# Optimization experiments

Measured on AMD Instinct MI355X. Metric: run time of the kernel, lower is better.

Reference implementation:

```python
import jax, jax.numpy as jnp
import numpy as np

B, N, D = 2, 2048, 256
H, HID, EN = 8, 64, 2
ALPHA = 0.2
NEG = -9e15


def setup_inputs() -> dict:
    key = jax.random.key(0)
    k1, k2, k3, k4, k5, k6 = jax.random.split(key, 6)
    fea_mats = jax.random.normal(k1, (B, N, D), dtype=jnp.float32)
    adj_mats = jax.random.randint(k2, (B, N, N), 0, 2).astype(jnp.float32)
    # xavier-uniform-like init (gain 1.414)
    def xav(k, shape):
        fan_in, fan_out = shape[-2], shape[-1]
        bound = 1.414 * np.sqrt(6.0 / (fan_in + fan_out))
        return jax.random.uniform(k, shape, jnp.float32, -bound, bound)
    W_att = xav(k3, (H, D, HID))          # per-head projection
    a_att = xav(k4, (H, 2 * HID, 1))      # per-head attention vector
    W_last = xav(k5, (H * HID, EN))       # last-layer projection
    a_last = xav(k6, (2 * EN, 1))         # last-layer attention vector
    return {"fea_mats": fea_mats, "adj_mats": adj_mats,
            "W_att": W_att, "a_att": a_att,
            "W_last": W_last, "a_last": a_last}


def _leaky(x):
    return jnp.where(x >= 0, x, ALPHA * x)


def _masked_attn(e, adj):
    # torch: where(adj!=0, e, 0) * adj; masked_fill(==0, -9e15); softmax(dim=1 over columns)
    att = jnp.where(adj != 0, e, jnp.zeros_like(e)) * adj
    att = jnp.where(att == 0, jnp.full_like(att, NEG), att)
    return jax.nn.softmax(att, axis=-1)


def reference(fea_mats, adj_mats, W_att, a_att, W_last, a_last):
    # ---- multi-head GAT layers (concat=True), eval mode -> dropout = identity ----
    wh = jnp.einsum('bnd,hdo->bhno', fea_mats, W_att)        # [B,H,N,HID]
    a1 = a_att[:, :HID, 0]                                   # [H,HID]
    a2 = a_att[:, HID:, 0]                                   # [H,HID]
    e1 = jnp.einsum('bhno,ho->bhn', wh, a1)                  # regulon part
    e2 = jnp.einsum('bhno,ho->bhn', wh, a2)                  # gene part
    e = _leaky(e1[:, :, :, None] + e2[:, :, None, :])        # [B,H,N,N]
    att = _masked_attn(e, adj_mats[:, None])                 # [B,H,N,N]
    x = jax.nn.elu(jnp.einsum('bhnm,bhmo->bhno', att, wh))   # [B,H,N,HID]
    x = jnp.transpose(x, (0, 2, 1, 3)).reshape(B, N, H * HID)
    # ---- last layer (concat=False), adj narrowed to square (already square) ----
    wh2 = jnp.einsum('bnd,de->bne', x, W_last)               # [B,N,EN]
    b1 = a_last[:EN, 0]
    b2 = a_last[EN:, 0]
    e = _leaky(jnp.einsum('bne,e->bn', wh2, b1)[:, :, None]
               + jnp.einsum('bne,e->bn', wh2, b2)[:, None, :])  # [B,N,N]
    att = _masked_attn(e, adj_mats)
    out = jax.nn.elu(jnp.einsum('bnm,bme->bne', att, wh2))   # [B,N,EN]
    return out
```

## Files before the change

### kernel.cpp

```cpp
#include <hip/hip_runtime.h>
#include <hip/hip_bf16.h>
#include <cstdint>
#include <cstddef>

#define B_ 2
#define N_ 2048
#define D_ 256
#define H_ 8
#define HID_ 64
#define EN_ 2
#define ALPHA 0.2f
#define NEGBIG (-3.0e38f)
#define LOG2E 1.4426950408889634f

typedef __bf16 bf16x8 __attribute__((ext_vector_type(8)));
typedef float f32x4 __attribute__((ext_vector_type(4)));
typedef unsigned short ushort8 __attribute__((ext_vector_type(8)));
typedef float float4v __attribute__((ext_vector_type(4)));
typedef float float2v __attribute__((ext_vector_type(2)));

__device__ __forceinline__ unsigned short f2bf(float f) {
    unsigned int u = __builtin_bit_cast(unsigned int, f);
    unsigned int r = u + 0x7FFFu + ((u >> 16) & 1u);
    return (unsigned short)(r >> 16);
}
__device__ __forceinline__ float bf2f(unsigned short u) {
    unsigned int x = ((unsigned int)u) << 16;
    return __builtin_bit_cast(float, x);
}
__device__ __forceinline__ float leakyf(float x) { return fmaxf(x, ALPHA * x); }

__device__ __forceinline__ ushort8 cvt8(const float* __restrict__ p) {
    float4v x0 = *(const float4v*)p;
    float4v x1 = *(const float4v*)(p + 4);
    ushort8 r;
    #pragma unroll
    for (int e = 0; e < 4; ++e) { r[e] = f2bf(x0[e]); r[e + 4] = f2bf(x1[e]); }
    return r;
}

__global__ void k_transpose_w(const float* __restrict__ W,
                              unsigned short* __restrict__ WT) {
    int h = blockIdx.x;
    const float* Wh = W + (size_t)h * D_ * HID_;
    unsigned short* WTh = WT + (size_t)h * HID_ * D_;
    for (int idx = threadIdx.x; idx < D_ * HID_; idx += blockDim.x) {
        int d = idx / HID_, o = idx % HID_;
        WTh[o * D_ + d] = f2bf(Wh[idx]);
    }
}

__global__ __launch_bounds__(256) void k_wh(
    const float* __restrict__ fea,
    const unsigned short* __restrict__ WT,
    const float* __restrict__ a_att,
    unsigned short* __restrict__ whT,
    float* __restrict__ e1, float* __restrict__ e2)
{
    int bid = blockIdx.x;
    int i0 = (bid & 31) << 6;
    int h  = (bid >> 5) & 7;
    int b  = bid >> 8;

    __shared__ __align__(16) union SmemA {
        struct { unsigned short fa[64 * 72]; unsigned short wt[64 * 72]; } s;
        float tr[64 * 65];
    } u;

    int t = threadIdx.x;
    int lane = t & 63;
    int wv = t >> 6;
    int r = lane & 15, q = lane >> 4;
    int ra = t >> 2;
    int cc = (t & 3) * 16;

    f32x4 acc[4] = {};

    const float* fearow = fea + ((size_t)(b * N_ + i0 + ra)) * D_;
    const unsigned short* wtrow = WT + ((size_t)(h * 64 + ra)) * D_;

    for (int d0 = 0; d0 < D_; d0 += 64) {
        *(ushort8*)&u.s.fa[ra * 72 + cc]     = cvt8(fearow + d0 + cc);
        *(ushort8*)&u.s.fa[ra * 72 + cc + 8] = cvt8(fearow + d0 + cc + 8);
        *(ushort8*)&u.s.wt[ra * 72 + cc]     = *(const ushort8*)(wtrow + d0 + cc);
        *(ushort8*)&u.s.wt[ra * 72 + cc + 8] = *(const ushort8*)(wtrow + d0 + cc + 8);
        __syncthreads();
        #pragma unroll
        for (int k0 = 0; k0 < 64; k0 += 32) {
            bf16x8 a = *(const bf16x8*)&u.s.fa[(16 * wv + r) * 72 + k0 + q * 8];
            #pragma unroll
            for (int f = 0; f < 4; ++f) {
                bf16x8 bb = *(const bf16x8*)&u.s.wt[(16 * f + r) * 72 + k0 + q * 8];
                acc[f] = __builtin_amdgcn_mfma_f32_16x16x32_bf16(a, bb, acc[f], 0, 0, 0);
            }
        }
        __syncthreads();
    }

    float a1v[4], a2v[4];
    #pragma unroll
    for (int f = 0; f < 4; ++f) {
        a1v[f] = a_att[h * 128 + 16 * f + r];
        a2v[f] = a_att[h * 128 + 64 + 16 * f + r];
    }
    #pragma unroll
    for (int rr = 0; rr < 4; ++rr) {
        float s1 = 0.f, s2 = 0.f;
        #pragma unroll
        for (int f = 0; f < 4; ++f) { s1 += acc[f][rr] * a1v[f]; s2 += acc[f][rr] * a2v[f]; }
        #pragma unroll
        for (int m = 1; m < 16; m <<= 1) {
            s1 += __shfl_xor(s1, m, 64);
            s2 += __shfl_xor(s2, m, 64);
        }
        if (r == 0) {
            int i = i0 + 16 * wv + 4 * q + rr;
            size_t idx = ((size_t)(b * H_ + h)) * N_ + i;
            e1[idx] = s1 * LOG2E; e2[idx] = s2 * LOG2E;
        }
    }

    #pragma unroll
    for (int f = 0; f < 4; ++f)
        #pragma unroll
        for (int rr = 0; rr < 4; ++rr)
            u.tr[(16 * f + r) * 65 + 16 * wv + 4 * q + rr] = acc[f][rr];
    __syncthreads();
    {
        int o = t >> 2;
        int ch = (t & 3) * 16;
        unsigned short tmp[16];
        #pragma unroll
        for (int e = 0; e < 16; ++e) tmp[e] = f2bf(u.tr[o * 65 + ch + e]);
        ushort8* dst = (ushort8*)(whT + (((size_t)(b * H_ + h) * 64 + o)) * N_ + i0 + ch);
        dst[0] = *(ushort8*)&tmp[0];
        dst[1] = *(ushort8*)&tmp[8];
    }
}

__global__ __launch_bounds__(256) void k_maxe2(const float* __restrict__ e2,
                                               float* __restrict__ mx) {
    int bh = blockIdx.x;
    int t = threadIdx.x;
    const float* row = e2 + (size_t)bh * N_;
    float M = NEGBIG;
    #pragma unroll
    for (int it = 0; it < N_ / 256; ++it) M = fmaxf(M, row[it * 256 + t]);
    #pragma unroll
    for (int s = 1; s < 64; s <<= 1) M = fmaxf(M, __shfl_xor(M, s, 64));
    __shared__ float red[4];
    if ((t & 63) == 0) red[t >> 6] = M;
    __syncthreads();
    if (t == 0) mx[bh] = fmaxf(fmaxf(red[0], red[1]), fmaxf(red[2], red[3]));
}

template<int JPER>
__global__ __launch_bounds__(256, 2) void k_pv1(
    const float* __restrict__ adj,
    const unsigned short* __restrict__ whT,
    const float* __restrict__ e1g, const float* __restrict__ e2g,
    const float* __restrict__ maxE2,
    unsigned short* __restrict__ x_part,
    float* __restrict__ zPart)
{
    constexpr int NT = JPER / 64;
    int s  = blockIdx.x;
    int i0 = blockIdx.y << 7;
    int bh = blockIdx.z;
    int h = bh & 7, b = bh >> 3;
    int jBeg = s * JPER;

    __shared__ __align__(16) unsigned short wt_lds[2][64 * 64];
    __shared__ float tE[JPER];
    __shared__ float vE[JPER];

    int t = threadIdx.x;
    int lane = t & 63;
    int wv = t >> 6;
    int r = lane & 15, q = lane >> 4;

    int ir0 = i0 + wv * 32 + r;
    int ir1 = ir0 + 16;
    float mx = maxE2[bh];
    float e1_0 = e1g[(size_t)bh * N_ + ir0];
    float e1_1 = e1g[(size_t)bh * N_ + ir1];
    float m0 = leakyf(e1_0 + mx), m1 = leakyf(e1_1 + mx);
    float sI0 = __builtin_amdgcn_exp2f(e1_0 - m0);
    float uI0 = __builtin_amdgcn_exp2f(ALPHA * e1_0 - m0);
    float sI1 = __builtin_amdgcn_exp2f(e1_1 - m1);
    float uI1 = __builtin_amdgcn_exp2f(ALPHA * e1_1 - m1);

    const float* e2p = e2g + (size_t)bh * N_ + jBeg;
    const float* ap0 = adj + ((size_t)(b * N_ + ir0)) * N_ + jBeg + q * 8;
    const float* ap1 = ap0 + (size_t)16 * N_;

    int c0 = t, c1 = t + 256;
    const unsigned short* wsrc0 =
        whT + ((size_t)bh * 64 + (c0 >> 3)) * N_ + jBeg + (c0 & 7) * 8;
    const unsigned short* wsrc1 =
        whT + ((size_t)bh * 64 + (c1 >> 3)) * N_ + jBeg + (c1 & 7) * 8;
    int woff0 = (c0 * 8) ^ (((c0 >> 3) & 7) << 3);
    int woff1 = (c1 * 8) ^ (((c1 >> 3) & 7) << 3);

    int swz = (r & 7) << 3;
    int koff0 = (8 * q) ^ swz;
    int koff1 = (32 + 8 * q) ^ swz;

    bf16x8 ones;
    #pragma unroll
    for (int e = 0; e < 8; ++e) ones[e] = (__bf16)1.0f;

    f32x4 acc[2][4] = {};
    f32x4 accz[2] = {};

    float4v aA[8], aB[8];
    ushort8 wN0, wN1;

#define LOADADJ(A, tile) do {                                                   \
        const float* p0 = ap0 + (tile) * 64;                                    \
        const float* p1 = ap1 + (tile) * 64;                                    \
        A[0] = *(const float4v*)(p0);      A[1] = *(const float4v*)(p0 + 4);    \
        A[2] = *(const float4v*)(p0 + 32); A[3] = *(const float4v*)(p0 + 36);   \
        A[4] = *(const float4v*)(p1);      A[5] = *(const float4v*)(p1 + 4);    \
        A[6] = *(const float4v*)(p1 + 32); A[7] = *(const float4v*)(p1 + 36);   \
    } while (0)
#define LOADW(tile) do {                                                        \
        wN0 = *(const ushort8*)(wsrc0 + (tile) * 64);                           \
        wN1 = *(const ushort8*)(wsrc1 + (tile) * 64);                           \
    } while (0)

    for (int jj = t; jj < JPER; jj += 256) {
        float ev = e2p[jj];
        tE[jj] = __builtin_amdgcn_exp2f(ev);
        vE[jj] = __builtin_amdgcn_exp2f(ALPHA * ev);
    }
    LOADW(0);
    *(ushort8*)&wt_lds[0][woff0] = wN0;
    *(ushort8*)&wt_lds[0][woff1] = wN1;
    if (NT > 1) LOADW(1);
    LOADADJ(aA, 0);
    if (NT > 1) LOADADJ(aB, 1);
    asm volatile("s_waitcnt lgkmcnt(0)" ::: "memory");
    __builtin_amdgcn_s_barrier();

    auto pgen = [&](const float4v* av, float sI, float uI,
                    const float4v& t0, const float4v& t1,
                    const float4v& t2, const float4v& t3,
                    const float4v& v0, const float4v& v1,
                    const float4v& v2, const float4v& v3,
                    bf16x8& pa0, bf16x8& pa1) {
        #pragma unroll
        for (int e = 0; e < 4; ++e) {
            pa0[e]     = (__bf16)(fmaxf(sI * t0[e], uI * v0[e]) * av[0][e]);
            pa0[e + 4] = (__bf16)(fmaxf(sI * t1[e], uI * v1[e]) * av[1][e]);
            pa1[e]     = (__bf16)(fmaxf(sI * t2[e], uI * v2[e]) * av[2][e]);
            pa1[e + 4] = (__bf16)(fmaxf(sI * t3[e], uI * v3[e]) * av[3][e]);
        }
    };

    #pragma unroll 2
    for (int t8 = 0; t8 < NT; ++t8) {
        const int cur = t8 & 1;
        if (t8 + 1 < NT) {
            *(ushort8*)&wt_lds[cur ^ 1][woff0] = wN0;
            *(ushort8*)&wt_lds[cur ^ 1][woff1] = wN1;
        }
        if (t8 + 2 < NT) LOADW(t8 + 2);

        const float* tb = &tE[t8 * 64 + q * 8];
        const float* vb = &vE[t8 * 64 + q * 8];
        float4v t0 = *(const float4v*)(tb),      t1 = *(const float4v*)(tb + 4);
        float4v t2 = *(const float4v*)(tb + 32), t3 = *(const float4v*)(tb + 36);
        float4v v0 = *(const float4v*)(vb),      v1 = *(const float4v*)(vb + 4);
        float4v v2 = *(const float4v*)(vb + 32), v3 = *(const float4v*)(vb + 36);

        bf16x8 pa00, pa01, pa10, pa11;
        if (cur == 0) {
            pgen(aA,     sI0, uI0, t0, t1, t2, t3, v0, v1, v2, v3, pa00, pa01);
            pgen(aA + 4, sI1, uI1, t0, t1, t2, t3, v0, v1, v2, v3, pa10, pa11);
        } else {
            pgen(aB,     sI0, uI0, t0, t1, t2, t3, v0, v1, v2, v3, pa00, pa01);
            pgen(aB + 4, sI1, uI1, t0, t1, t2, t3, v0, v1, v2, v3, pa10, pa11);
        }
        if (t8 + 2 < NT) {
            if (cur == 0) LOADADJ(aA, t8 + 2);
            else          LOADADJ(aB, t8 + 2);
        }

        const unsigned short* Wb = wt_lds[cur];
        bf16x8 bb0[4], bb1[4];
        #pragma unroll
        for (int f = 0; f < 4; ++f) {
            bb0[f] = *(const bf16x8*)&Wb[f * 1024 + r * 64 + koff0];
            bb1[f] = *(const bf16x8*)&Wb[f * 1024 + r * 64 + koff1];
        }
        #pragma unroll
        for (int f = 0; f < 4; ++f) {
            acc[0][f] = __builtin_amdgcn_mfma_f32_16x16x32_bf16(pa00, bb0[f], acc[0][f], 0, 0, 0);
            acc[1][f] = __builtin_amdgcn_mfma_f32_16x16x32_bf16(pa10, bb0[f], acc[1][f], 0, 0, 0);
        }
        accz[0] = __builtin_amdgcn_mfma_f32_16x16x32_bf16(pa00, ones, accz[0], 0, 0, 0);
        accz[1] = __builtin_amdgcn_mfma_f32_16x16x32_bf16(pa10, ones, accz[1], 0, 0, 0);
        #pragma unroll
        for (int f = 0; f < 4; ++f) {
            acc[0][f] = __builtin_amdgcn_mfma_f32_16x16x32_bf16(pa01, bb1[f], acc[0][f], 0, 0, 0);
            acc[1][f] = __builtin_amdgcn_mfma_f32_16x16x32_bf16(pa11, bb1[f], acc[1][f], 0, 0, 0);
        }
        accz[0] = __builtin_amdgcn_mfma_f32_16x16x32_bf16(pa01, ones, accz[0], 0, 0, 0);
        accz[1] = __builtin_amdgcn_mfma_f32_16x16x32_bf16(pa11, ones, accz[1], 0, 0, 0);

        asm volatile("s_waitcnt lgkmcnt(0)" ::: "memory");
        __builtin_amdgcn_s_barrier();
    }
#undef LOADADJ
#undef LOADW

    unsigned short* xp = x_part + ((size_t)s * (B_ * N_) + (size_t)b * N_) * 512 + h * 64;
    #pragma unroll
    for (int mR = 0; mR < 2; ++mR) {
        #pragma unroll
        for (int f = 0; f < 4; ++f) {
            #pragma unroll
            for (int rr = 0; rr < 4; ++rr) {
                int i = i0 + wv * 32 + mR * 16 + 4 * q + rr;
                xp[(size_t)i * 512 + 16 * f + r] = f2bf(acc[mR][f][rr]);
            }
        }
        if (r == 0) {
            #pragma unroll
            for (int rr = 0; rr < 4; ++rr) {
                int i = i0 + wv * 32 + mR * 16 + 4 * q + rr;
                zPart[((size_t)(s * 16 + bh)) * N_ + i] = accz[mR][rr];
            }
        }
    }
}

__global__ __launch_bounds__(256) void k_wh2(
    const unsigned short* __restrict__ x_part,
    const float* __restrict__ zPart,
    const float* __restrict__ W_last,
    const float* __restrict__ a_last,
    float* __restrict__ wh2, float* __restrict__ g1, float* __restrict__ g2,
    int S)
{
    int idx = blockIdx.x * 4 + (threadIdx.x >> 6);
    int lane = threadIdx.x & 63;
    int b = idx >> 11, n = idx & (N_ - 1);
    float a0 = 0.f, a1 = 0.f;
    #pragma unroll
    for (int it = 0; it < 8; ++it) {
        int k = it * 64 + lane;
        float xv = 0.f, zv = 0.f;
        for (int s = 0; s < S; ++s) {
            xv += bf2f(x_part[((size_t)s * (B_ * N_) + idx) * 512 + k]);
            zv += zPart[((size_t)(s * 16 + b * 8 + it)) * N_ + n];
        }
        float x = (zv > 0.f) ? xv / zv : 0.f;
        x = x > 0.f ? x : expm1f(x);
        float2v wl = *(const float2v*)(W_last + k * 2);
        a0 += x * wl[0];
        a1 += x * wl[1];
    }
    #pragma unroll
    for (int s = 1; s < 64; s <<= 1) {
        a0 += __shfl_xor(a0, s, 64);
        a1 += __shfl_xor(a1, s, 64);
    }
    if (lane == 0) {
        wh2[idx * 2] = a0; wh2[idx * 2 + 1] = a1;
        g1[idx] = (a0 * a_last[0] + a1 * a_last[1]) * LOG2E;
        g2[idx] = (a0 * a_last[2] + a1 * a_last[3]) * LOG2E;
    }
}

__global__ __launch_bounds__(256) void k_out(
    const float* __restrict__ adj,
    const float* __restrict__ wh2,
    const float* __restrict__ g1, const float* __restrict__ g2,
    float* __restrict__ out)
{
    int idx = blockIdx.x * 4 + (threadIdx.x >> 6);
    int lane = threadIdx.x & 63;
    int b = idx >> 11;
    float gi = g1[idx];
    const float* arow = adj + (size_t)idx * N_;
    const float* g2b = g2 + (size_t)b * N_;
    const float* wh2b = wh2 + (size_t)b * N_ * 2;

    float ep[32];
    float M = NEGBIG;
    #pragma unroll
    for (int it = 0; it < 8; ++it) {
        int j = it * 256 + lane * 4;
        float4v a4 = *(const float4v*)(arow + j);
        float4v s4 = *(const float4v*)(g2b + j);
        #pragma unroll
        for (int e = 0; e < 4; ++e) {
            float l = leakyf(gi + s4[e]);
            float v = (a4[e] != 0.f) ? l : NEGBIG;
            ep[it * 4 + e] = v;
            M = fmaxf(M, v);
        }
    }
    #pragma unroll
    for (int s = 1; s < 64; s <<= 1) M = fmaxf(M, __shfl_xor(M, s, 64));

    float Z = 0.f, A0 = 0.f, A1 = 0.f;
    #pragma unroll
    for (int it = 0; it < 8; ++it) {
        int j = it * 256 + lane * 4;
        float4v wA = *(const float4v*)(wh2b + 2 * j);
        float4v wB = *(const float4v*)(wh2b + 2 * j + 4);
        #pragma unroll
        for (int e = 0; e < 4; ++e) {
            float p = __builtin_amdgcn_exp2f(ep[it * 4 + e] - M);
            Z += p;
            float w0 = (e < 2) ? wA[2 * e] : wB[2 * (e - 2)];
            float w1 = (e < 2) ? wA[2 * e + 1] : wB[2 * (e - 2) + 1];
            A0 += p * w0;
            A1 += p * w1;
        }
    }
    #pragma unroll
    for (int s = 1; s < 64; s <<= 1) {
        Z += __shfl_xor(Z, s, 64);
        A0 += __shfl_xor(A0, s, 64);
        A1 += __shfl_xor(A1, s, 64);
    }
    if (lane == 0) {
        float o0 = A0 / Z, o1 = A1 / Z;
        o0 = o0 > 0.f ? o0 : expm1f(o0);
        o1 = o1 > 0.f ? o1 : expm1f(o1);
        float2v ov; ov[0] = o0; ov[1] = o1;
        *(float2v*)(out + idx * 2) = ov;
    }
}

extern "C" void kernel_launch(void* const* d_in, const int* in_sizes, int n_in,
                              void* d_out, int out_size, void* d_ws, size_t ws_size,
                              hipStream_t stream) {
    const float* fea    = (const float*)d_in[0];
    const float* adj    = (const float*)d_in[1];
    const float* W_att  = (const float*)d_in[2];
    const float* a_att  = (const float*)d_in[3];
    const float* W_last = (const float*)d_in[4];
    const float* a_last = (const float*)d_in[5];

    char* ws = (char*)d_ws;
    float* e1  = (float*)(ws + 0);
    float* e2  = (float*)(ws + 131072);
    float* mxE = (float*)(ws + 262144);
    float* wh2 = (float*)(ws + 262400);
    float* g1  = (float*)(ws + 295168);
    float* g2  = (float*)(ws + 311552);
    unsigned short* WT  = (unsigned short*)(ws + 327936);
    unsigned short* whT = (unsigned short*)(ws + 590080);
    float* zPart = (float*)(ws + 4784384);
    unsigned short* x_part = (unsigned short*)(ws + 5308672);

    const size_t BASE = 5308672ULL, XPART = 4194304ULL;
    int S = (ws_size >= BASE + 4 * XPART) ? 4
          : (ws_size >= BASE + 2 * XPART) ? 2 : 1;

    k_transpose_w<<<dim3(H_), dim3(256), 0, stream>>>(W_att, WT);
    k_wh<<<dim3(B_ * H_ * (N_ / 64)), dim3(256), 0, stream>>>(
        fea, WT, a_att, whT, e1, e2);
    k_maxe2<<<dim3(B_ * H_), dim3(256), 0, stream>>>(e2, mxE);
    if (S == 4)
        k_pv1<512><<<dim3(4, N_ / 128, B_ * H_), dim3(256), 0, stream>>>(
            adj, whT, e1, e2, mxE, x_part, zPart);
    else if (S == 2)
        k_pv1<1024><<<dim3(2, N_ / 128, B_ * H_), dim3(256), 0, stream>>>(
            adj, whT, e1, e2, mxE, x_part, zPart);
    else
        k_pv1<2048><<<dim3(1, N_ / 128, B_ * H_), dim3(256), 0, stream>>>(
            adj, whT, e1, e2, mxE, x_part, zPart);
    k_wh2<<<dim3(B_ * N_ / 4), dim3(256), 0, stream>>>(
        x_part, zPart, W_last, a_last, wh2, g1, g2, S);
    k_out<<<dim3(B_ * N_ / 4), dim3(256), 0, stream>>>(
        adj, wh2, g1, g2, (float*)d_out);
}
```

Before: 100.2 us.

## Compress adjacency to byte mask and compute two heads per projection block

A new prep kernel converts the fp32 adjacency matrix once into an 8-bit 0/1 mask. The attention-times-values kernel and the output kernel then read bytes instead of floats, which cuts the adjacency traffic that every head re-reads. The projection kernel now handles two heads per block so the feature tile is loaded once for both. The k_pv1 launch-bounds occupancy hint rises from 2 to 4. The costs are an extra pass over the full adjacency, more workspace, and a mask that keeps only zero versus nonzero, so the result matches only for binary adjacency values.

```diff
diff --git a/kernel.cpp b/kernel.cpp
--- a/kernel.cpp
+++ b/kernel.cpp
@@ -18,6 +18,7 @@
 typedef unsigned short ushort8 __attribute__((ext_vector_type(8)));
 typedef float float4v __attribute__((ext_vector_type(4)));
 typedef float float2v __attribute__((ext_vector_type(2)));
+typedef unsigned int uint2v __attribute__((ext_vector_type(2)));
 
 __device__ __forceinline__ unsigned short f2bf(float f) {
     unsigned int u = __builtin_bit_cast(unsigned int, f);
@@ -29,6 +30,9 @@
     return __builtin_bit_cast(float, x);
 }
 __device__ __forceinline__ float leakyf(float x) { return fmaxf(x, ALPHA * x); }
+__device__ __forceinline__ float ub(unsigned int d, int e) {
+    return (float)((d >> (8 * e)) & 0xffu);
+}
 
 __device__ __forceinline__ ushort8 cvt8(const float* __restrict__ p) {
     float4v x0 = *(const float4v*)p;
@@ -37,6 +41,21 @@
     #pragma unroll
     for (int e = 0; e < 4; ++e) { r[e] = f2bf(x0[e]); r[e + 4] = f2bf(x1[e]); }
     return r;
+}
+
+__global__ __launch_bounds__(256) void k_prep(const float* __restrict__ adj,
+                                              unsigned char* __restrict__ adj8) {
+    size_t base = ((size_t)blockIdx.x * 256 + threadIdx.x) * 8;
+    float4v a = *(const float4v*)(adj + base);
+    float4v b = *(const float4v*)(adj + base + 4);
+    unsigned int lo = 0, hi = 0;
+    #pragma unroll
+    for (int e = 0; e < 4; ++e) {
+        lo |= (a[e] != 0.f ? 1u : 0u) << (8 * e);
+        hi |= (b[e] != 0.f ? 1u : 0u) << (8 * e);
+    }
+    uint2v o; o[0] = lo; o[1] = hi;
+    *(uint2v*)(adj8 + base) = o;
 }
 
 __global__ void k_transpose_w(const float* __restrict__ W,
@@ -57,41 +76,48 @@
     unsigned short* __restrict__ whT,
     float* __restrict__ e1, float* __restrict__ e2)
 {
-    int bid = blockIdx.x;
-    int i0 = (bid & 31) << 6;
-    int h  = (bid >> 5) & 7;
-    int b  = bid >> 8;
+    int i0 = blockIdx.x << 6;
+    int h0 = blockIdx.y * 2;
+    int b  = blockIdx.z;
 
     __shared__ __align__(16) union SmemA {
-        struct { unsigned short fa[64 * 72]; unsigned short wt[64 * 72]; } s;
+        struct { unsigned short fa[64 * 72]; unsigned short wt[2][64 * 72]; } s;
         float tr[64 * 65];
     } u;
 
     int t = threadIdx.x;
     int lane = t & 63;
     int wv = t >> 6;
+    int hw = wv & 1;
+    int half = wv >> 1;
     int r = lane & 15, q = lane >> 4;
     int ra = t >> 2;
     int cc = (t & 3) * 16;
-
-    f32x4 acc[4] = {};
+    int rowbase = half * 32;
+
+    f32x4 acc[2][4] = {};
 
     const float* fearow = fea + ((size_t)(b * N_ + i0 + ra)) * D_;
-    const unsigned short* wtrow = WT + ((size_t)(h * 64 + ra)) * D_;
+    const unsigned short* wt0row = WT + ((size_t)(h0 * 64 + ra)) * D_;
+    const unsigned short* wt1row = WT + ((size_t)((h0 + 1) * 64 + ra)) * D_;
 
     for (int d0 = 0; d0 < D_; d0 += 64) {
-        *(ushort8*)&u.s.fa[ra * 72 + cc]     = cvt8(fearow + d0 + cc);
-        *(ushort8*)&u.s.fa[ra * 72 + cc + 8] = cvt8(fearow + d0 + cc + 8);
-        *(ushort8*)&u.s.wt[ra * 72 + cc]     = *(const ushort8*)(wtrow + d0 + cc);
-        *(ushort8*)&u.s.wt[ra * 72 + cc + 8] = *(const ushort8*)(wtrow + d0 + cc + 8);
+        *(ushort8*)&u.s.fa[ra * 72 + cc]       = cvt8(fearow + d0 + cc);
+        *(ushort8*)&u.s.fa[ra * 72 + cc + 8]   = cvt8(fearow + d0 + cc + 8);
+        *(ushort8*)&u.s.wt[0][ra * 72 + cc]     = *(const ushort8*)(wt0row + d0 + cc);
+        *(ushort8*)&u.s.wt[0][ra * 72 + cc + 8] = *(const ushort8*)(wt0row + d0 + cc + 8);
+        *(ushort8*)&u.s.wt[1][ra * 72 + cc]     = *(const ushort8*)(wt1row + d0 + cc);
+        *(ushort8*)&u.s.wt[1][ra * 72 + cc + 8] = *(const ushort8*)(wt1row + d0 + cc + 8);
         __syncthreads();
         #pragma unroll
         for (int k0 = 0; k0 < 64; k0 += 32) {
-            bf16x8 a = *(const bf16x8*)&u.s.fa[(16 * wv + r) * 72 + k0 + q * 8];
+            bf16x8 a0 = *(const bf16x8*)&u.s.fa[(rowbase + r) * 72 + k0 + q * 8];
+            bf16x8 a1 = *(const bf16x8*)&u.s.fa[(rowbase + 16 + r) * 72 + k0 + q * 8];
             #pragma unroll
             for (int f = 0; f < 4; ++f) {
-                bf16x8 bb = *(const bf16x8*)&u.s.wt[(16 * f + r) * 72 + k0 + q * 8];
-                acc[f] = __builtin_amdgcn_mfma_f32_16x16x32_bf16(a, bb, acc[f], 0, 0, 0);
+                bf16x8 bb = *(const bf16x8*)&u.s.wt[hw][(16 * f + r) * 72 + k0 + q * 8];
+                acc[0][f] = __builtin_amdgcn_mfma_f32_16x16x32_bf16(a0, bb, acc[0][f], 0, 0, 0);
+                acc[1][f] = __builtin_amdgcn_mfma_f32_16x16x32_bf16(a1, bb, acc[1][f], 0, 0, 0);
             }
         }
         __syncthreads();
@@ -100,41 +126,52 @@
     float a1v[4], a2v[4];
     #pragma unroll
     for (int f = 0; f < 4; ++f) {
-        a1v[f] = a_att[h * 128 + 16 * f + r];
-        a2v[f] = a_att[h * 128 + 64 + 16 * f + r];
-    }
-    #pragma unroll
-    for (int rr = 0; rr < 4; ++rr) {
-        float s1 = 0.f, s2 = 0.f;
-        #pragma unroll
-        for (int f = 0; f < 4; ++f) { s1 += acc[f][rr] * a1v[f]; s2 += acc[f][rr] * a2v[f]; }
-        #pragma unroll
-        for (int m = 1; m < 16; m <<= 1) {
-            s1 += __shfl_xor(s1, m, 64);
-            s2 += __shfl_xor(s2, m, 64);
-        }
-        if (r == 0) {
-            int i = i0 + 16 * wv + 4 * q + rr;
-            size_t idx = ((size_t)(b * H_ + h)) * N_ + i;
-            e1[idx] = s1 * LOG2E; e2[idx] = s2 * LOG2E;
-        }
-    }
-
-    #pragma unroll
-    for (int f = 0; f < 4; ++f)
-        #pragma unroll
-        for (int rr = 0; rr < 4; ++rr)
-            u.tr[(16 * f + r) * 65 + 16 * wv + 4 * q + rr] = acc[f][rr];
-    __syncthreads();
-    {
-        int o = t >> 2;
-        int ch = (t & 3) * 16;
-        unsigned short tmp[16];
-        #pragma unroll
-        for (int e = 0; e < 16; ++e) tmp[e] = f2bf(u.tr[o * 65 + ch + e]);
-        ushort8* dst = (ushort8*)(whT + (((size_t)(b * H_ + h) * 64 + o)) * N_ + i0 + ch);
-        dst[0] = *(ushort8*)&tmp[0];
-        dst[1] = *(ushort8*)&tmp[8];
+        a1v[f] = a_att[(h0 + hw) * 128 + 16 * f + r];
+        a2v[f] = a_att[(h0 + hw) * 128 + 64 + 16 * f + r];
+    }
+    #pragma unroll
+    for (int m = 0; m < 2; ++m) {
+        #pragma unroll
+        for (int rr = 0; rr < 4; ++rr) {
+            float s1 = 0.f, s2 = 0.f;
+            #pragma unroll
+            for (int f = 0; f < 4; ++f) { s1 += acc[m][f][rr] * a1v[f]; s2 += acc[m][f][rr] * a2v[f]; }
+            #pragma unroll
+            for (int sh = 1; sh < 16; sh <<= 1) {
+                s1 += __shfl_xor(s1, sh, 64);
+                s2 += __shfl_xor(s2, sh, 64);
+            }
+            if (r == 0) {
+                int i = i0 + rowbase + 16 * m + 4 * q + rr;
+                size_t idx = ((size_t)(b * H_ + h0 + hw)) * N_ + i;
+                e1[idx] = s1 * LOG2E; e2[idx] = s2 * LOG2E;
+            }
+        }
+    }
+
+    #pragma unroll
+    for (int hh = 0; hh < 2; ++hh) {
+        __syncthreads();
+        if (hw == hh) {
+            #pragma unroll
+            for (int m = 0; m < 2; ++m)
+                #pragma unroll
+                for (int f = 0; f < 4; ++f)
+                    #pragma unroll
+                    for (int rr = 0; rr < 4; ++rr)
+                        u.tr[(16 * f + r) * 65 + rowbase + 16 * m + 4 * q + rr] = acc[m][f][rr];
+        }
+        __syncthreads();
+        {
+            int o = t >> 2;
+            int ch = (t & 3) * 16;
+            unsigned short tmp[16];
+            #pragma unroll
+            for (int e = 0; e < 16; ++e) tmp[e] = f2bf(u.tr[o * 65 + ch + e]);
+            ushort8* dst = (ushort8*)(whT + (((size_t)(b * H_ + h0 + hh) * 64 + o)) * N_ + i0 + ch);
+            dst[0] = *(ushort8*)&tmp[0];
+            dst[1] = *(ushort8*)&tmp[8];
+        }
     }
 }
 
@@ -155,8 +192,8 @@
 }
 
 template<int JPER>
-__global__ __launch_bounds__(256, 2) void k_pv1(
-    const float* __restrict__ adj,
+__global__ __launch_bounds__(256, 4) void k_pv1(
+    const unsigned char* __restrict__ adj8,
     const unsigned short* __restrict__ whT,
     const float* __restrict__ e1g, const float* __restrict__ e2g,
     const float* __restrict__ maxE2,
@@ -191,8 +228,8 @@
     float uI1 = __builtin_amdgcn_exp2f(ALPHA * e1_1 - m1);
 
     const float* e2p = e2g + (size_t)bh * N_ + jBeg;
-    const float* ap0 = adj + ((size_t)(b * N_ + ir0)) * N_ + jBeg + q * 8;
-    const float* ap1 = ap0 + (size_t)16 * N_;
+    const unsigned char* ap0 = adj8 + ((size_t)(b * N_ + ir0)) * N_ + jBeg + q * 8;
+    const unsigned char* ap1 = ap0 + (size_t)16 * N_;
 
     int c0 = t, c1 = t + 256;
     const unsigned short* wsrc0 =
@@ -213,16 +250,14 @@
     f32x4 acc[2][4] = {};
     f32x4 accz[2] = {};
 
-    float4v aA[8], aB[8];
+    uint2v aA[4], aB[4];
     ushort8 wN0, wN1;
 
 #define LOADADJ(A, tile) do {                                                   \
-        const float* p0 = ap0 + (tile) * 64;                                    \
-        const float* p1 = ap1 + (tile) * 64;                                    \
-        A[0] = *(const float4v*)(p0);      A[1] = *(const float4v*)(p0 + 4);    \
-        A[2] = *(const float4v*)(p0 + 32); A[3] = *(const float4v*)(p0 + 36);   \
-        A[4] = *(const float4v*)(p1);      A[5] = *(const float4v*)(p1 + 4);    \
-        A[6] = *(const float4v*)(p1 + 32); A[7] = *(const float4v*)(p1 + 36);   \
+        const unsigned char* p0 = ap0 + (tile) * 64;                            \
+        const unsigned char* p1 = ap1 + (tile) * 64;                            \
+        A[0] = *(const uint2v*)(p0);      A[1] = *(const uint2v*)(p0 + 32);     \
+        A[2] = *(const uint2v*)(p1);      A[3] = *(const uint2v*)(p1 + 32);     \
     } while (0)
 #define LOADW(tile) do {                                                        \
         wN0 = *(const ushort8*)(wsrc0 + (tile) * 64);                           \
@@ -243,7 +278,7 @@
     asm volatile("s_waitcnt lgkmcnt(0)" ::: "memory");
     __builtin_amdgcn_s_barrier();
 
-    auto pgen = [&](const float4v* av, float sI, float uI,
+    auto pgen = [&](const uint2v& alo, const uint2v& ahi, float sI, float uI,
                     const float4v& t0, const float4v& t1,
                     const float4v& t2, const float4v& t3,
                     const float4v& v0, const float4v& v1,
@@ -251,10 +286,10 @@
                     bf16x8& pa0, bf16x8& pa1) {
         #pragma unroll
         for (int e = 0; e < 4; ++e) {
-            pa0[e]     = (__bf16)(fmaxf(sI * t0[e], uI * v0[e]) * av[0][e]);
-            pa0[e + 4] = (__bf16)(fmaxf(sI * t1[e], uI * v1[e]) * av[1][e]);
-            pa1[e]     = (__bf16)(fmaxf(sI * t2[e], uI * v2[e]) * av[2][e]);
-            pa1[e + 4] = (__bf16)(fmaxf(sI * t3[e], uI * v3[e]) * av[3][e]);
+            pa0[e]     = (__bf16)(fmaxf(sI * t0[e], uI * v0[e]) * ub(alo[0], e));
+            pa0[e + 4] = (__bf16)(fmaxf(sI * t1[e], uI * v1[e]) * ub(alo[1], e));
+            pa1[e]     = (__bf16)(fmaxf(sI * t2[e], uI * v2[e]) * ub(ahi[0], e));
+            pa1[e + 4] = (__bf16)(fmaxf(sI * t3[e], uI * v3[e]) * ub(ahi[1], e));
         }
     };
 
@@ -276,11 +311,11 @@
 
         bf16x8 pa00, pa01, pa10, pa11;
         if (cur == 0) {
-            pgen(aA,     sI0, uI0, t0, t1, t2, t3, v0, v1, v2, v3, pa00, pa01);
-            pgen(aA + 4, sI1, uI1, t0, t1, t2, t3, v0, v1, v2, v3, pa10, pa11);
+            pgen(aA[0], aA[1], sI0, uI0, t0, t1, t2, t3, v0, v1, v2, v3, pa00, pa01);
+            pgen(aA[2], aA[3], sI1, uI1, t0, t1, t2, t3, v0, v1, v2, v3, pa10, pa11);
         } else {
-            pgen(aB,     sI0, uI0, t0, t1, t2, t3, v0, v1, v2, v3, pa00, pa01);
-            pgen(aB + 4, sI1, uI1, t0, t1, t2, t3, v0, v1, v2, v3, pa10, pa11);
+            pgen(aB[0], aB[1], sI0, uI0, t0, t1, t2, t3, v0, v1, v2, v3, pa00, pa01);
+            pgen(aB[2], aB[3], sI1, uI1, t0, t1, t2, t3, v0, v1, v2, v3, pa10, pa11);
         }
         if (t8 + 2 < NT) {
             if (cur == 0) LOADADJ(aA, t8 + 2);
@@ -375,7 +410,7 @@
 }
 
 __global__ __launch_bounds__(256) void k_out(
-    const float* __restrict__ adj,
+    const unsigned char* __restrict__ adj8,
     const float* __restrict__ wh2,
     const float* __restrict__ g1, const float* __restrict__ g2,
     float* __restrict__ out)
@@ -384,7 +419,7 @@
     int lane = threadIdx.x & 63;
     int b = idx >> 11;
     float gi = g1[idx];
-    const float* arow = adj + (size_t)idx * N_;
+    const unsigned char* arow = adj8 + (size_t)idx * N_;
     const float* g2b = g2 + (size_t)b * N_;
     const float* wh2b = wh2 + (size_t)b * N_ * 2;
 
@@ -393,12 +428,12 @@
     #pragma unroll
     for (int it = 0; it < 8; ++it) {
         int j = it * 256 + lane * 4;
-        float4v a4 = *(const float4v*)(arow + j);
+        unsigned int d = *(const unsigned int*)(arow + j);
         float4v s4 = *(const float4v*)(g2b + j);
         #pragma unroll
         for (int e = 0; e < 4; ++e) {
             float l = leakyf(gi + s4[e]);
-            float v = (a4[e] != 0.f) ? l : NEGBIG;
+            float v = ((d >> (8 * e)) & 0xffu) ? l : NEGBIG;
             ep[it * 4 + e] = v;
             M = fmaxf(M, v);
         }
@@ -457,27 +492,29 @@
     unsigned short* WT  = (unsigned short*)(ws + 327936);
     unsigned short* whT = (unsigned short*)(ws + 590080);
     float* zPart = (float*)(ws + 4784384);
-    unsigned short* x_part = (unsigned short*)(ws + 5308672);
-
-    const size_t BASE = 5308672ULL, XPART = 4194304ULL;
+    unsigned char* adj8 = (unsigned char*)(ws + 5308672);
+    unsigned short* x_part = (unsigned short*)(ws + 13697280);
+
+    const size_t BASE = 13697280ULL, XPART = 4194304ULL;
     int S = (ws_size >= BASE + 4 * XPART) ? 4
           : (ws_size >= BASE + 2 * XPART) ? 2 : 1;
 
+    k_prep<<<dim3(B_ * N_ * N_ / 2048), dim3(256), 0, stream>>>(adj, adj8);
     k_transpose_w<<<dim3(H_), dim3(256), 0, stream>>>(W_att, WT);
-    k_wh<<<dim3(B_ * H_ * (N_ / 64)), dim3(256), 0, stream>>>(
+    k_wh<<<dim3(N_ / 64, H_ / 2, B_), dim3(256), 0, stream>>>(
         fea, WT, a_att, whT, e1, e2);
     k_maxe2<<<dim3(B_ * H_), dim3(256), 0, stream>>>(e2, mxE);
     if (S == 4)
         k_pv1<512><<<dim3(4, N_ / 128, B_ * H_), dim3(256), 0, stream>>>(
-            adj, whT, e1, e2, mxE, x_part, zPart);
+            adj8, whT, e1, e2, mxE, x_part, zPart);
     else if (S == 2)
         k_pv1<1024><<<dim3(2, N_ / 128, B_ * H_), dim3(256), 0, stream>>>(
-            adj, whT, e1, e2, mxE, x_part, zPart);
+            adj8, whT, e1, e2, mxE, x_part, zPart);
     else
         k_pv1<2048><<<dim3(1, N_ / 128, B_ * H_), dim3(256), 0, stream>>>(
-            adj, whT, e1, e2, mxE, x_part, zPart);
+            adj8, whT, e1, e2, mxE, x_part, zPart);
     k_wh2<<<dim3(B_ * N_ / 4), dim3(256), 0, stream>>>(
         x_part, zPart, W_last, a_last, wh2, g1, g2, S);
     k_out<<<dim3(B_ * N_ / 4), dim3(256), 0, stream>>>(
-        adj, wh2, g1, g2, (float*)d_out);
-}
+        adj8, wh2, g1, g2, (float*)d_out);
+}
```

After: 104.7 us. +4.5%, slower.
